# Kernel tuning notes

Hardware: AMD Instinct MI355X
Metric: run time of the kernel (lower is better)

The kernel has to match this reference:

```python
import jax, jax.numpy as jnp
import numpy as np

# NAM: in_features independent 1->H->H->1 MLPs (FeatureNNs), batched over the
# feature dimension F instead of a Python loop of tiny kernels.
# inputs: (B, F); W1,b1: (F, H); W2: (F, H, H); b2: (F, H); W3: (F, H); b3: (F,)

def setup_inputs() -> dict:
    key = jax.random.key(0)
    ks = jax.random.split(key, 7)
    B, F, H = 8192, 128, 64
    s1 = 1.0  # fan_in = 1 for first layer
    s2 = 1.0 / np.sqrt(H)
    return {
        "inputs": jax.random.normal(ks[0], (B, F), dtype=jnp.float32),
        "W1": jax.random.normal(ks[1], (F, H), dtype=jnp.float32) * s1,
        "b1": jax.random.normal(ks[2], (F, H), dtype=jnp.float32) * 0.01,
        "W2": jax.random.normal(ks[3], (F, H, H), dtype=jnp.float32) * s2,
        "b2": jax.random.normal(ks[4], (F, H), dtype=jnp.float32) * 0.01,
        "W3": jax.random.normal(ks[5], (F, H), dtype=jnp.float32) * s2,
        "b3": jax.random.normal(ks[6], (F,), dtype=jnp.float32) * 0.01,
    }


def reference(inputs, W1, b1, W2, b2, W3, b3):
    # Layer 1: scalar input per feature -> hidden.  (B,F,1)*(F,H) -> (B,F,H)
    h1 = jax.nn.relu(inputs[:, :, None] * W1[None, :, :] + b1[None, :, :])
    # Layer 2: per-feature hidden->hidden batched matmul.
    h2 = jax.nn.relu(jnp.einsum("bfh,fhk->bfk", h1, W2) + b2[None, :, :])
    # Output layer: hidden -> scalar per feature.
    fnn = jnp.einsum("bfh,fh->bf", h2, W3) + b3[None, :]  # (B, F)
    out = fnn.sum(axis=-1)  # (B,)  additive model output
    return (out, fnn)
```

## Files before the change

### kernel.cpp

```cpp
#include <hip/hip_runtime.h>

#define B 8192
#define F 128
#define H 64

typedef __attribute__((ext_vector_type(8))) short bf16x8;
typedef __attribute__((ext_vector_type(4))) float f32x4;

static __device__ __forceinline__ unsigned short f32_to_bf16_rne(float v) {
    unsigned int u = __float_as_uint(v);
    unsigned int r = (u + 0x7FFFu + ((u >> 16) & 1u)) >> 16;
    return (unsigned short)r;
}
static __device__ __forceinline__ float bf16_to_f32(unsigned short h) {
    return __uint_as_float(((unsigned int)h) << 16);
}


__global__ __launch_bounds__(256) void w2_pack(const float* __restrict__ W2,
                                               bf16x8* __restrict__ ws)
{
    const int f = blockIdx.x;
    const int tid = threadIdx.x;
    const float* W2f = W2 + (size_t)f * H * H;
#pragma unroll
    for (int t = tid; t < 512; t += 256) {
        const int n = t & 63;
        const int g = t >> 6;
        const int nt = n >> 4, c = n & 15;
        const int ks = g >> 2, q = g & 3;
        const int slot = (nt * 2 + ks) * 64 + c + 16 * q;
        bf16x8 hv, lv;
#pragma unroll
        for (int jj = 0; jj < 8; ++jj) {
            const float wv = W2f[(g * 8 + jj) * H + n];
            const unsigned short hi = f32_to_bf16_rne(wv);
            const unsigned short lo = f32_to_bf16_rne(wv - bf16_to_f32(hi));
            hv[jj] = (short)hi;
            lv[jj] = (short)lo;
        }
        ws[((size_t)f * 2 + 0) * 512 + slot] = hv;
        ws[((size_t)f * 2 + 1) * 512 + slot] = lv;
    }
}

__global__ __launch_bounds__(256, 2) void nam_main_ws(
    const float* __restrict__ inputs, const float* __restrict__ W1,
    const float* __restrict__ b1, const bf16x8* __restrict__ wsb,
    const float* __restrict__ b2, const float* __restrict__ W3,
    const float* __restrict__ b3, float* __restrict__ out,
    float* __restrict__ fnn_out)
{
    const int tid = threadIdx.x;
    const int f = blockIdx.y;
    const int b0 = blockIdx.x * 256;

    const int lane = tid & 63;
    const int w    = tid >> 6;
    const int q    = lane >> 4;
    const int col  = lane & 15;

    bf16x8 bhi[4][2], blo[4][2];
#pragma unroll
    for (int nt = 0; nt < 4; ++nt)
#pragma unroll
        for (int ks = 0; ks < 2; ++ks) {
            const int slot = (nt * 2 + ks) * 64 + lane;
            bhi[nt][ks] = wsb[((size_t)f * 2 + 0) * 512 + slot];
            blo[nt][ks] = wsb[((size_t)f * 2 + 1) * 512 + slot];
        }

    const float* W1f = W1 + f * H;
    const float* b1f = b1 + f * H;
    const float* b2f = b2 + f * H;
    const float* W3f = W3 + f * H;

    float w1v[16], b1v[16];
#pragma unroll
    for (int ks = 0; ks < 2; ++ks)
#pragma unroll
        for (int j4 = 0; j4 < 2; ++j4) {
            const float4 wv = *(const float4*)&W1f[ks * 32 + q * 8 + j4 * 4];
            const float4 bv = *(const float4*)&b1f[ks * 32 + q * 8 + j4 * 4];
            w1v[ks * 8 + j4 * 4 + 0] = wv.x; w1v[ks * 8 + j4 * 4 + 1] = wv.y;
            w1v[ks * 8 + j4 * 4 + 2] = wv.z; w1v[ks * 8 + j4 * 4 + 3] = wv.w;
            b1v[ks * 8 + j4 * 4 + 0] = bv.x; b1v[ks * 8 + j4 * 4 + 1] = bv.y;
            b1v[ks * 8 + j4 * 4 + 2] = bv.z; b1v[ks * 8 + j4 * 4 + 3] = bv.w;
        }
    float b2v[4], w3v[4];
#pragma unroll
    for (int nt = 0; nt < 4; ++nt) {
        b2v[nt] = b2f[nt * 16 + col];
        w3v[nt] = W3f[nt * 16 + col];
    }
    const float b3f = b3[f];

    float x4[4];
#pragma unroll
    for (int mt = 0; mt < 4; ++mt)
        x4[mt] = inputs[(size_t)(b0 + w * 64 + mt * 16 + col) * F + f];

#pragma unroll
    for (int mt = 0; mt < 4; ++mt) {
        const int rbase = b0 + w * 64 + mt * 16;
        const float x = x4[mt];

        f32x4 acc[4];
#pragma unroll
        for (int nt = 0; nt < 4; ++nt) {
            acc[nt][0] = b2v[nt]; acc[nt][1] = b2v[nt];
            acc[nt][2] = b2v[nt]; acc[nt][3] = b2v[nt];
        }

#pragma unroll
        for (int ks = 0; ks < 2; ++ks) {
            union { unsigned int u[4]; bf16x8 v; } Ah, Al;
#pragma unroll
            for (int t = 0; t < 4; ++t) {
                const float r0 = fmaxf(fmaf(x, w1v[ks * 8 + 2 * t],     b1v[ks * 8 + 2 * t]),     0.0f);
                const float r1 = fmaxf(fmaf(x, w1v[ks * 8 + 2 * t + 1], b1v[ks * 8 + 2 * t + 1]), 0.0f);
                const unsigned int u0 = __float_as_uint(r0);
                const unsigned int u1 = __float_as_uint(r1);
                const float l0 = r0 - __uint_as_float(u0 & 0xFFFF0000u);
                const float l1 = r1 - __uint_as_float(u1 & 0xFFFF0000u);
                Ah.u[t] = __builtin_amdgcn_perm(u1, u0, 0x07060302);
                Al.u[t] = __builtin_amdgcn_perm(__float_as_uint(l1),
                                                __float_as_uint(l0), 0x07060302);
            }
#pragma unroll
            for (int nt = 0; nt < 4; ++nt) {
                acc[nt] = __builtin_amdgcn_mfma_f32_16x16x32_bf16(Ah.v, bhi[nt][ks], acc[nt], 0, 0, 0);
                acc[nt] = __builtin_amdgcn_mfma_f32_16x16x32_bf16(Ah.v, blo[nt][ks], acc[nt], 0, 0, 0);
                acc[nt] = __builtin_amdgcn_mfma_f32_16x16x32_bf16(Al.v, bhi[nt][ks], acc[nt], 0, 0, 0);
            }
        }

        float s[4];
#pragma unroll
        for (int reg = 0; reg < 4; ++reg) {
            float t = 0.0f;
#pragma unroll
            for (int nt = 0; nt < 4; ++nt)
                t = fmaf(fmaxf(acc[nt][reg], 0.0f), w3v[nt], t);
            s[reg] = t;
        }
#pragma unroll
        for (int m_ = 1; m_ <= 8; m_ <<= 1)
#pragma unroll
            for (int reg = 0; reg < 4; ++reg)
                s[reg] += __shfl_xor(s[reg], m_, 64);
        if (col == 0) {
#pragma unroll
            for (int reg = 0; reg < 4; ++reg) {
                const int row = rbase + 4 * q + reg;
                const float val = s[reg] + b3f;
                fnn_out[(size_t)row * F + f] = val;
                atomicAdd(&out[row], val);
            }
        }
    }
}

__global__ __launch_bounds__(256, 3) void nam_main_lds(
    const float* __restrict__ inputs, const float* __restrict__ W1,
    const float* __restrict__ b1, const float* __restrict__ W2,
    const float* __restrict__ b2, const float* __restrict__ W3,
    const float* __restrict__ b3, float* __restrict__ out,
    float* __restrict__ fnn_out)
{
    const int tid = threadIdx.x;
    const int f = blockIdx.y;
    const int b0 = blockIdx.x * 256;

    const float* W1f = W1 + f * H;
    const float* b1f = b1 + f * H;
    const float* W2f = W2 + (size_t)f * H * H;
    const float* b2f = b2 + f * H;
    const float* W3f = W3 + f * H;

    __shared__ short bhi_s[512 * 8];
    __shared__ short blo_s[512 * 8];

#pragma unroll
    for (int t = tid; t < 512; t += 256) {
        const int n = t & 63, g = t >> 6;
        const int nt = n >> 4, c = n & 15;
        const int ks = g >> 2, q = g & 3;
        const int slot = (nt * 2 + ks) * 64 + c + 16 * q;
        bf16x8 hv, lv;
#pragma unroll
        for (int jj = 0; jj < 8; ++jj) {
            const float wv = W2f[(g * 8 + jj) * H + n];
            const unsigned short hi = f32_to_bf16_rne(wv);
            const unsigned short lo = f32_to_bf16_rne(wv - bf16_to_f32(hi));
            hv[jj] = (short)hi;
            lv[jj] = (short)lo;
        }
        *(bf16x8*)&bhi_s[slot * 8] = hv;
        *(bf16x8*)&blo_s[slot * 8] = lv;
    }

    const int lane = tid & 63, w = tid >> 6;
    const int q = lane >> 4, col = lane & 15;

    float w1v[16], b1v[16];
#pragma unroll
    for (int ks = 0; ks < 2; ++ks)
#pragma unroll
        for (int j = 0; j < 8; ++j) {
            w1v[ks * 8 + j] = W1f[ks * 32 + q * 8 + j];
            b1v[ks * 8 + j] = b1f[ks * 32 + q * 8 + j];
        }
    float b2v[4], w3v[4];
#pragma unroll
    for (int nt = 0; nt < 4; ++nt) {
        b2v[nt] = b2f[nt * 16 + col];
        w3v[nt] = W3f[nt * 16 + col];
    }
    const float b3f = b3[f];

    float x4[4];
#pragma unroll
    for (int mt = 0; mt < 4; ++mt)
        x4[mt] = inputs[(size_t)(b0 + w * 64 + mt * 16 + col) * F + f];

    __syncthreads();

    bf16x8 bhi[4][2], blo[4][2];
#pragma unroll
    for (int nt = 0; nt < 4; ++nt)
#pragma unroll
        for (int ks = 0; ks < 2; ++ks) {
            const int slot = (nt * 2 + ks) * 64 + lane;
            bhi[nt][ks] = *(bf16x8*)&bhi_s[slot * 8];
            blo[nt][ks] = *(bf16x8*)&blo_s[slot * 8];
        }

#pragma unroll 1
    for (int mt = 0; mt < 4; ++mt) {
        const int rbase = b0 + w * 64 + mt * 16;
        const float x = x4[mt];

        f32x4 acc[4];
#pragma unroll
        for (int nt = 0; nt < 4; ++nt) {
            acc[nt][0] = b2v[nt]; acc[nt][1] = b2v[nt];
            acc[nt][2] = b2v[nt]; acc[nt][3] = b2v[nt];
        }
#pragma unroll
        for (int ks = 0; ks < 2; ++ks) {
            union { unsigned int u[4]; bf16x8 v; } Ah, Al;
#pragma unroll
            for (int t = 0; t < 4; ++t) {
                const float r0 = fmaxf(fmaf(x, w1v[ks * 8 + 2 * t],     b1v[ks * 8 + 2 * t]),     0.0f);
                const float r1 = fmaxf(fmaf(x, w1v[ks * 8 + 2 * t + 1], b1v[ks * 8 + 2 * t + 1]), 0.0f);
                const unsigned int u0 = __float_as_uint(r0);
                const unsigned int u1 = __float_as_uint(r1);
                const float l0 = r0 - __uint_as_float(u0 & 0xFFFF0000u);
                const float l1 = r1 - __uint_as_float(u1 & 0xFFFF0000u);
                Ah.u[t] = __builtin_amdgcn_perm(u1, u0, 0x07060302);
                Al.u[t] = __builtin_amdgcn_perm(__float_as_uint(l1),
                                                __float_as_uint(l0), 0x07060302);
            }
#pragma unroll
            for (int nt = 0; nt < 4; ++nt) {
                acc[nt] = __builtin_amdgcn_mfma_f32_16x16x32_bf16(Ah.v, bhi[nt][ks], acc[nt], 0, 0, 0);
                acc[nt] = __builtin_amdgcn_mfma_f32_16x16x32_bf16(Ah.v, blo[nt][ks], acc[nt], 0, 0, 0);
                acc[nt] = __builtin_amdgcn_mfma_f32_16x16x32_bf16(Al.v, bhi[nt][ks], acc[nt], 0, 0, 0);
            }
        }
        float s[4];
#pragma unroll
        for (int reg = 0; reg < 4; ++reg) {
            float t = 0.0f;
#pragma unroll
            for (int nt = 0; nt < 4; ++nt)
                t = fmaf(fmaxf(acc[nt][reg], 0.0f), w3v[nt], t);
            s[reg] = t;
        }
#pragma unroll
        for (int m_ = 1; m_ <= 8; m_ <<= 1)
#pragma unroll
            for (int reg = 0; reg < 4; ++reg)
                s[reg] += __shfl_xor(s[reg], m_, 64);
        if (col == 0) {
#pragma unroll
            for (int reg = 0; reg < 4; ++reg) {
                const int row = rbase + 4 * q + reg;
                const float val = s[reg] + b3f;
                fnn_out[(size_t)row * F + f] = val;
                atomicAdd(&out[row], val);
            }
        }
    }
}

extern "C" void kernel_launch(void* const* d_in, const int* in_sizes, int n_in,
                              void* d_out, int out_size, void* d_ws, size_t ws_size,
                              hipStream_t stream) {
    const float* inputs = (const float*)d_in[0];
    const float* W1     = (const float*)d_in[1];
    const float* b1     = (const float*)d_in[2];
    const float* W2     = (const float*)d_in[3];
    const float* b2     = (const float*)d_in[4];
    const float* W3     = (const float*)d_in[5];
    const float* b3     = (const float*)d_in[6];

    float* out = (float*)d_out;
    float* fnn = out + B;

    hipMemsetAsync(out, 0, B * sizeof(float), stream);

    const size_t ws_needed = (size_t)F * 2 * 512 * sizeof(bf16x8);
    if (ws_size >= ws_needed) {
        bf16x8* wsb = (bf16x8*)d_ws;
        w2_pack<<<dim3(F), 256, 0, stream>>>(W2, wsb);
        nam_main_ws<<<dim3(B / 256, F), 256, 0, stream>>>(
            inputs, W1, b1, wsb, b2, W3, b3, out, fnn);
    } else {
        nam_main_lds<<<dim3(B / 256, F), 256, 0, stream>>>(
            inputs, W1, b1, W2, b2, W3, b3, out, fnn);
    }
}
```

Measured before the change: 113.8 us.

## Split hidden columns across wave pairs to cut registers and raise occupancy

```diff
diff --git a/kernel.cpp b/kernel.cpp
--- a/kernel.cpp
+++ b/kernel.cpp
@@ -44,7 +44,7 @@
     }
 }
 
-__global__ __launch_bounds__(256, 2) void nam_main_ws(
+__global__ __launch_bounds__(256, 4) void nam_main(
     const float* __restrict__ inputs, const float* __restrict__ W1,
     const float* __restrict__ b1, const bf16x8* __restrict__ wsb,
     const float* __restrict__ b2, const float* __restrict__ W3,
@@ -57,23 +57,25 @@
 
     const int lane = tid & 63;
     const int w    = tid >> 6;
+    const int pair = w >> 1;
+    const int half = w & 1;
     const int q    = lane >> 4;
     const int col  = lane & 15;
-
-    bf16x8 bhi[4][2], blo[4][2];
-#pragma unroll
-    for (int nt = 0; nt < 4; ++nt)
+    const int rw   = b0 + pair * 128;
+
+    bf16x8 bh[2][2], bl[2][2];
+#pragma unroll
+    for (int j = 0; j < 2; ++j)
 #pragma unroll
         for (int ks = 0; ks < 2; ++ks) {
+            const int nt = half * 2 + j;
             const int slot = (nt * 2 + ks) * 64 + lane;
-            bhi[nt][ks] = wsb[((size_t)f * 2 + 0) * 512 + slot];
-            blo[nt][ks] = wsb[((size_t)f * 2 + 1) * 512 + slot];
+            bh[j][ks] = wsb[(size_t)f * 1024 + slot];
+            bl[j][ks] = wsb[(size_t)f * 1024 + 512 + slot];
         }
 
     const float* W1f = W1 + f * H;
     const float* b1f = b1 + f * H;
-    const float* b2f = b2 + f * H;
-    const float* W3f = W3 + f * H;
 
     float w1v[16], b1v[16];
 #pragma unroll
@@ -87,29 +89,30 @@
             b1v[ks * 8 + j4 * 4 + 0] = bv.x; b1v[ks * 8 + j4 * 4 + 1] = bv.y;
             b1v[ks * 8 + j4 * 4 + 2] = bv.z; b1v[ks * 8 + j4 * 4 + 3] = bv.w;
         }
-    float b2v[4], w3v[4];
-#pragma unroll
-    for (int nt = 0; nt < 4; ++nt) {
-        b2v[nt] = b2f[nt * 16 + col];
-        w3v[nt] = W3f[nt * 16 + col];
-    }
-    const float b3f = b3[f];
-
-    float x4[4];
-#pragma unroll
-    for (int mt = 0; mt < 4; ++mt)
-        x4[mt] = inputs[(size_t)(b0 + w * 64 + mt * 16 + col) * F + f];
-
-#pragma unroll
-    for (int mt = 0; mt < 4; ++mt) {
-        const int rbase = b0 + w * 64 + mt * 16;
-        const float x = x4[mt];
-
-        f32x4 acc[4];
-#pragma unroll
-        for (int nt = 0; nt < 4; ++nt) {
-            acc[nt][0] = b2v[nt]; acc[nt][1] = b2v[nt];
-            acc[nt][2] = b2v[nt]; acc[nt][3] = b2v[nt];
+
+    float b2v[2], w3v[2];
+#pragma unroll
+    for (int j = 0; j < 2; ++j) {
+        const int nt = half * 2 + j;
+        b2v[j] = b2[f * H + nt * 16 + col];
+        w3v[j] = W3[f * H + nt * 16 + col];
+    }
+    const float b3h = (half == 0) ? b3[f] : 0.0f;
+
+    float xc = inputs[(size_t)(rw + col) * F + f];
+
+#pragma unroll 1
+    for (int mt = 0; mt < 8; ++mt) {
+        float xn = 0.0f;
+        if (mt < 7)
+            xn = inputs[(size_t)(rw + (mt + 1) * 16 + col) * F + f];
+        const float x = xc;
+
+        f32x4 acc[2];
+#pragma unroll
+        for (int j = 0; j < 2; ++j) {
+            acc[j][0] = b2v[j]; acc[j][1] = b2v[j];
+            acc[j][2] = b2v[j]; acc[j][3] = b2v[j];
         }
 
 #pragma unroll
@@ -128,10 +131,10 @@
                                                 __float_as_uint(l0), 0x07060302);
             }
 #pragma unroll
-            for (int nt = 0; nt < 4; ++nt) {
-                acc[nt] = __builtin_amdgcn_mfma_f32_16x16x32_bf16(Ah.v, bhi[nt][ks], acc[nt], 0, 0, 0);
-                acc[nt] = __builtin_amdgcn_mfma_f32_16x16x32_bf16(Ah.v, blo[nt][ks], acc[nt], 0, 0, 0);
-                acc[nt] = __builtin_amdgcn_mfma_f32_16x16x32_bf16(Al.v, bhi[nt][ks], acc[nt], 0, 0, 0);
+            for (int j = 0; j < 2; ++j) {
+                acc[j] = __builtin_amdgcn_mfma_f32_16x16x32_bf16(Ah.v, bh[j][ks], acc[j], 0, 0, 0);
+                acc[j] = __builtin_amdgcn_mfma_f32_16x16x32_bf16(Ah.v, bl[j][ks], acc[j], 0, 0, 0);
+                acc[j] = __builtin_amdgcn_mfma_f32_16x16x32_bf16(Al.v, bh[j][ks], acc[j], 0, 0, 0);
             }
         }
 
@@ -140,8 +143,8 @@
         for (int reg = 0; reg < 4; ++reg) {
             float t = 0.0f;
 #pragma unroll
-            for (int nt = 0; nt < 4; ++nt)
-                t = fmaf(fmaxf(acc[nt][reg], 0.0f), w3v[nt], t);
+            for (int j = 0; j < 2; ++j)
+                t = fmaf(fmaxf(acc[j][reg], 0.0f), w3v[j], t);
             s[reg] = t;
         }
 #pragma unroll
@@ -152,12 +155,13 @@
         if (col == 0) {
 #pragma unroll
             for (int reg = 0; reg < 4; ++reg) {
-                const int row = rbase + 4 * q + reg;
-                const float val = s[reg] + b3f;
-                fnn_out[(size_t)row * F + f] = val;
+                const int row = rw + mt * 16 + 4 * q + reg;
+                const float val = s[reg] + b3h;
+                atomicAdd(&fnn_out[(size_t)row * F + f], val);
                 atomicAdd(&out[row], val);
             }
         }
+        xc = xn;
     }
 }
 
@@ -178,8 +182,8 @@
     const float* b2f = b2 + f * H;
     const float* W3f = W3 + f * H;
 
-    __shared__ short bhi_s[512 * 8];
-    __shared__ short blo_s[512 * 8];
+    __shared__ bf16x8 bhi_s[512];
+    __shared__ bf16x8 blo_s[512];
 
 #pragma unroll
     for (int t = tid; t < 512; t += 256) {
@@ -196,8 +200,8 @@
             hv[jj] = (short)hi;
             lv[jj] = (short)lo;
         }
-        *(bf16x8*)&bhi_s[slot * 8] = hv;
-        *(bf16x8*)&blo_s[slot * 8] = lv;
+        bhi_s[slot] = hv;
+        blo_s[slot] = lv;
     }
 
     const int lane = tid & 63, w = tid >> 6;
@@ -232,8 +236,8 @@
 #pragma unroll
         for (int ks = 0; ks < 2; ++ks) {
             const int slot = (nt * 2 + ks) * 64 + lane;
-            bhi[nt][ks] = *(bf16x8*)&bhi_s[slot * 8];
-            blo[nt][ks] = *(bf16x8*)&blo_s[slot * 8];
+            bhi[nt][ks] = bhi_s[slot];
+            blo[nt][ks] = blo_s[slot];
         }
 
 #pragma unroll 1
@@ -309,15 +313,15 @@
     float* out = (float*)d_out;
     float* fnn = out + B;
 
-    hipMemsetAsync(out, 0, B * sizeof(float), stream);
-
     const size_t ws_needed = (size_t)F * 2 * 512 * sizeof(bf16x8);
     if (ws_size >= ws_needed) {
+        hipMemsetAsync(d_out, 0, (size_t)out_size * sizeof(float), stream);
         bf16x8* wsb = (bf16x8*)d_ws;
         w2_pack<<<dim3(F), 256, 0, stream>>>(W2, wsb);
-        nam_main_ws<<<dim3(B / 256, F), 256, 0, stream>>>(
+        nam_main<<<dim3(B / 256, F), 256, 0, stream>>>(
             inputs, W1, b1, wsb, b2, W3, b3, out, fnn);
     } else {
+        hipMemsetAsync(out, 0, B * sizeof(float), stream);
         nam_main_lds<<<dim3(B / 256, F), 256, 0, stream>>>(
             inputs, W1, b1, W2, b2, W3, b3, out, fnn);
     }
```

New measurement: 209.9 us. 84.5% more time.
